# Optimization experiments

Measured on AMD Instinct MI355X. Metric: run time of the kernel, lower is better.

The kernel has to match this reference:

```python
import jax, jax.numpy as jnp
import numpy as np

B, NPG, NFEAT, NHID, NCLASS = 32, 256, 128, 64, 6
N = B * NPG
E_PER = NPG * 16
C = 1.0
SQC = 1.0  # sqrt(c)
MIN_NORM = 1e-15
PROJ_EPS = 4e-3
LAMB = 1.0


def _norm(x):
    return jnp.clip(jnp.linalg.norm(x, axis=-1, keepdims=True), MIN_NORM)


def artanh(x):
    x = jnp.clip(x, -1.0 + 1e-7, 1.0 - 1e-7)
    return 0.5 * (jnp.log1p(x) - jnp.log1p(-x))


def proj(x):
    # clip points to stay inside the Poincare ball
    n = _norm(x)
    maxn = (1.0 - PROJ_EPS) / SQC
    return jnp.where(n > maxn, x / n * maxn, x)


def expmap0(u):
    un = _norm(u)
    return jnp.tanh(SQC * un) * u / (SQC * un)


def logmap0(p):
    pn = _norm(p)
    return artanh(SQC * pn) * p / (SQC * pn)


def mobius_matvec(W, x):
    xn = _norm(x)
    mx = x @ W.T
    mxn = _norm(mx)
    return jnp.tanh(mxn / xn * artanh(SQC * xn)) * mx / (mxn * SQC)


def mobius_add(x, y):
    x2 = jnp.sum(x * x, -1, keepdims=True)
    y2 = jnp.sum(y * y, -1, keepdims=True)
    xy = jnp.sum(x * y, -1, keepdims=True)
    num = (1.0 + 2.0 * C * xy + C * y2) * x + (1.0 - C * x2) * y
    den = 1.0 + 2.0 * C * xy + C * C * x2 * y2
    return num / jnp.clip(den, MIN_NORM)


def hgc_layer(xh, adj, W, b):
    # HypLinear (mobius matvec + hyperbolic bias)
    h = proj(mobius_matvec(W, xh))
    hb = proj(expmap0(b.reshape(1, -1)))
    h = proj(mobius_add(h, hb))
    # HypAgg: aggregate in tangent space at origin
    h = proj(expmap0(adj @ logmap0(h)))
    # HypAct: relu in tangent space
    return proj(expmap0(jax.nn.relu(logmap0(h))))


def hgpsl_pool(x, adj, att, nb, npg):
    deg = adj.sum(-1)
    dis = jnp.where(deg > 0, deg ** -0.5, 0.0)
    prop = dis[:, None] * (adj @ (dis[:, None] * x))
    score = jnp.abs(x - prop).sum(-1)  # [N]
    k = npg // 2
    vals, idx = jax.lax.top_k(score.reshape(nb, npg), k)  # per-graph top-k
    gidx = (idx + (jnp.arange(nb) * npg)[:, None]).reshape(-1)  # global ids
    xn = x[gidx] * jnp.tanh(vals).reshape(-1, 1)
    adj_ind = adj[gidx][:, gidx]
    # structure learning: single-head additive attention, masked per graph
    d = xn.shape[-1]
    e = jax.nn.leaky_relu((xn @ att[:d])[:, None] + (xn @ att[d:])[None, :], 0.2)
    gid = jnp.repeat(jnp.arange(nb), k)
    mask = gid[:, None] == gid[None, :]
    new_adj = jnp.where(mask, jax.nn.relu(e) + LAMB * adj_ind, 0.0)
    return xn, new_adj


def readout(x, nb, k):
    xr = x.reshape(nb, k, -1)
    return jnp.concatenate([xr.max(axis=1), xr.mean(axis=1)], axis=-1)


def to_hyp(t):
    return proj(expmap0(t))  # proj_tan0 is identity on the Poincare ball


def forward(x, edge_index, W1, b1, W2, b2, W3, b3, att1, att2,
            lw1, lb1, lw2, lb2, lw3, lb3):
    row, col = edge_index[0], edge_index[1]
    w = (x[row].sum(-1) + x[col].sum(-1)) * 0.5
    adj1 = jnp.zeros((N, N), x.dtype).at[row, col].set(w)

    t = logmap0(hgc_layer(to_hyp(x), adj1, W1, b1))
    t, adj2 = hgpsl_pool(t, adj1, att1, B, NPG)
    k1 = NPG // 2
    x1 = readout(t, B, k1)

    t = logmap0(hgc_layer(to_hyp(t), adj2, W2, b2))
    t, adj3 = hgpsl_pool(t, adj2, att2, B, k1)
    k2 = k1 // 2
    x2 = readout(t, B, k2)

    t = logmap0(hgc_layer(to_hyp(t), adj3, W3, b3))
    x3 = readout(t, B, k2)

    r = jax.nn.relu(x1) + jax.nn.relu(x2) + jax.nn.relu(x3)
    r = jax.nn.relu(r @ lw1.T + lb1)
    r = jax.nn.relu(r @ lw2.T + lb2)
    return jax.nn.log_softmax(r @ lw3.T + lb3, axis=-1)


def setup_inputs() -> dict:
    key = jax.random.key(0)
    ks = jax.random.split(key, 16)
    s = 0.1
    x = jax.random.normal(ks[0], (N, NFEAT), jnp.float32)
    off = jnp.repeat(jnp.arange(B, dtype=jnp.int32) * NPG, E_PER)
    row = jax.random.randint(ks[1], (B * E_PER,), 0, NPG, jnp.int32) + off
    col = jax.random.randint(ks[2], (B * E_PER,), 0, NPG, jnp.int32) + off
    edge_index = jnp.stack([row, col])
    return {
        "x": x,
        "edge_index": edge_index,
        "W1": jax.random.normal(ks[3], (NHID, NFEAT), jnp.float32) * s,
        "b1": jax.random.normal(ks[4], (NHID,), jnp.float32) * s,
        "W2": jax.random.normal(ks[5], (NHID, NHID), jnp.float32) * s,
        "b2": jax.random.normal(ks[6], (NHID,), jnp.float32) * s,
        "W3": jax.random.normal(ks[7], (NHID, NHID), jnp.float32) * s,
        "b3": jax.random.normal(ks[8], (NHID,), jnp.float32) * s,
        "att1": jax.random.normal(ks[9], (2 * NHID,), jnp.float32) * s,
        "att2": jax.random.normal(ks[10], (2 * NHID,), jnp.float32) * s,
        "lw1": jax.random.normal(ks[11], (NHID, 2 * NHID), jnp.float32) * s,
        "lb1": jnp.zeros((NHID,), jnp.float32),
        "lw2": jax.random.normal(ks[12], (NHID // 2, NHID), jnp.float32) * s,
        "lb2": jnp.zeros((NHID // 2,), jnp.float32),
        "lw3": jax.random.normal(ks[13], (NCLASS, NHID // 2), jnp.float32) * s,
        "lb3": jnp.zeros((NCLASS,), jnp.float32),
    }


def reference(x, edge_index, W1, b1, W2, b2, W3, b3, att1, att2,
              lw1, lb1, lw2, lb2, lw3, lb3):
    return forward(x, edge_index, W1, b1, W2, b2, W3, b3, att1, att2,
                   lw1, lb1, lw2, lb2, lw3, lb3)
```

## Files before the change

kernel.cpp:

```cpp
#include <hip/hip_runtime.h>
#include <math.h>

#define MAXN 0.996f

__device__ __forceinline__ float wredsum(float v) {
#pragma unroll
  for (int o = 32; o > 0; o >>= 1) v += __shfl_xor(v, o);
  return v;
}

__device__ __forceinline__ float artanh_f(float x) {
  x = fminf(fmaxf(x, -1.0f + 1e-7f), 1.0f - 1e-7f);
  return 0.5f * (log1pf(x) - log1pf(-x));
}

__global__ void k_rowsum(const float* __restrict__ x, float* __restrict__ s) {
  const int row = blockIdx.x, j = threadIdx.x;
  float a = x[(size_t)row * 128 + j] + x[(size_t)row * 128 + 64 + j];
  a = wredsum(a);
  if (j == 0) s[row] = a;
}

__global__ void k_edges(const int* __restrict__ er, const int* __restrict__ ec,
                        const float* __restrict__ s, float* __restrict__ adj, int nE) {
  int e = blockIdx.x * blockDim.x + threadIdx.x;
  if (e >= nE) return;
  int r = er[e], c = ec[e];
  int g = r >> 8;
  adj[(((size_t)g * 256) + (r & 255)) * 256 + (c & 255)] = 0.5f * (s[r] + s[c]);
}

template <int IND>
__global__ void k_stageA(const float* __restrict__ x, const float* __restrict__ Wm,
                         const float* __restrict__ b, float* __restrict__ u) {
  const int row = blockIdx.x;
  const int j = threadIdx.x;
  __shared__ float xs[IND];
  for (int t = j; t < IND; t += 64) xs[t] = x[(size_t)row * IND + t];
  __syncthreads();

  float bj = b[j];
  float nb = sqrtf(wredsum(bj * bj));
  float ub = fmaxf(nb, 1e-15f);
  float eb = tanhf(ub) / ub;
  float cb = fmaxf(eb * nb, 1e-15f);
  float hbj = bj * eb * ((cb > MAXN) ? MAXN / cb : 1.0f);
  float y2 = wredsum(hbj * hbj);

  float a2 = 0.f;
  for (int t = j; t < IND; t += 64) a2 += xs[t] * xs[t];
  float nx = sqrtf(wredsum(a2));
  float un = fmaxf(nx, 1e-15f);
  float s1 = tanhf(un) / un;
  float nv = s1 * nx;
  float nn = fmaxf(nv, 1e-15f);
  float s2 = (nn > MAXN) ? MAXN / nn : 1.0f;
  float alpha = s1 * s2;
  float xn = fmaxf(fminf(nn, MAXN), 1e-15f);

  float y = 0.f;
  const float* wr = Wm + (size_t)j * IND;
  for (int t = 0; t < IND; ++t) y += xs[t] * wr[t];
  float mxj = alpha * y;
  float mxn = fmaxf(sqrtf(wredsum(mxj * mxj)), 1e-15f);
  float hj = (tanhf(mxn / xn * artanh_f(xn)) / mxn) * mxj;

  float hn = fmaxf(sqrtf(wredsum(hj * hj)), 1e-15f);
  if (hn > MAXN) hj *= MAXN / hn;

  float x2 = wredsum(hj * hj);
  float xy = wredsum(hj * hbj);
  float num = (1.f + 2.f * xy + y2) * hj + (1.f - x2) * hbj;
  float den = fmaxf(1.f + 2.f * xy + x2 * y2, 1e-15f);
  float aj = num / den;

  float an = fmaxf(sqrtf(wredsum(aj * aj)), 1e-15f);
  float pn = an;
  if (an > MAXN) { aj *= MAXN / an; pn = MAXN; }
  u[(size_t)row * 64 + j] = (artanh_f(pn) / pn) * aj;
}

template <int NPGL>
__global__ void k_stageB(const float* __restrict__ adj, const float* __restrict__ u,
                         float* __restrict__ t, float* __restrict__ dis, int wantDis) {
  const int row = blockIdx.x;
  const int g = row / NPGL;
  const int j = threadIdx.x;
  const float* arow = adj + (size_t)row * NPGL;
  const float* ug = u + (size_t)g * NPGL * 64;
  float acc = 0.f, dsum = 0.f;
  for (int c = 0; c < NPGL; ++c) { float a = arow[c]; acc += a * ug[(size_t)c * 64 + j]; dsum += a; }

  float n0 = sqrtf(wredsum(acc * acc));
  float u0 = fmaxf(n0, 1e-15f);
  float e1 = tanhf(u0) / u0;
  float c1 = fmaxf(e1 * n0, 1e-15f);
  float v = acc * e1;
  if (c1 > MAXN) { v *= MAXN / c1; c1 = MAXN; }
  v *= artanh_f(c1) / c1;
  v = fmaxf(v, 0.f);

  float n2 = sqrtf(wredsum(v * v));
  float u2 = fmaxf(n2, 1e-15f);
  float e2 = tanhf(u2) / u2;
  float c2 = fmaxf(e2 * n2, 1e-15f);
  v *= e2;
  if (c2 > MAXN) { v *= MAXN / c2; c2 = MAXN; }
  v *= artanh_f(c2) / c2;
  t[(size_t)row * 64 + j] = v;
  if (wantDis && j == 0) dis[row] = (dsum > 0.f) ? (1.0f / sqrtf(dsum)) : 0.f;
}

template <int NPGL>
__global__ void k_stageC(const float* __restrict__ adj, const float* __restrict__ t,
                         const float* __restrict__ dis, float* __restrict__ score) {
  const int row = blockIdx.x;
  const int g = row / NPGL;
  const int j = threadIdx.x;
  const float* arow = adj + (size_t)row * NPGL;
  const float* tg = t + (size_t)g * NPGL * 64;
  const float* dg = dis + (size_t)g * NPGL;
  float acc = 0.f;
  for (int c = 0; c < NPGL; ++c) acc += arow[c] * dg[c] * tg[(size_t)c * 64 + j];
  float d = fabsf(t[(size_t)row * 64 + j] - dis[row] * acc);
  d = wredsum(d);
  if (j == 0) score[row] = d;
}

template <int NPGL>
__global__ void k_stageD(const float* __restrict__ score, const float* __restrict__ t,
                         const float* __restrict__ att, float* __restrict__ xn,
                         float* __restrict__ s1o, float* __restrict__ s2o,
                         int* __restrict__ gidx, float* __restrict__ xread) {
  constexpr int K = NPGL / 2;
  const int g = blockIdx.x;
  const int i = threadIdx.x;
  __shared__ float sc[NPGL];
  __shared__ int sel[K];
  __shared__ float sval[K];
  __shared__ float xs[K * 64];
  sc[i] = score[(size_t)g * NPGL + i];
  __syncthreads();
  float si = sc[i];
  int rank = 0;
  for (int c = 0; c < NPGL; ++c) { float v = sc[c]; rank += (v > si) || (v == si && c < i); }
  if (rank < K) { sel[rank] = i; sval[rank] = si; }
  __syncthreads();
  if (i < K) {
    int li = sel[i];
    float tv = tanhf(sval[i]);
    const float* trow = t + ((size_t)g * NPGL + li) * 64;
    float a = 0.f, b = 0.f;
    for (int jj = 0; jj < 64; ++jj) {
      float v = trow[jj] * tv;
      xs[i * 64 + jj] = v;
      a += v * att[jj];
      b += v * att[64 + jj];
    }
    s1o[(size_t)g * K + i] = a;
    s2o[(size_t)g * K + i] = b;
    gidx[(size_t)g * K + i] = li;
    float* xout = xn + ((size_t)g * K + i) * 64;
    for (int jj = 0; jj < 64; ++jj) xout[jj] = xs[i * 64 + jj];
  }
  __syncthreads();
  if (i < 64) {
    float mx = -1e30f, sm = 0.f;
    for (int r = 0; r < K; ++r) { float v = xs[r * 64 + i]; mx = fmaxf(mx, v); sm += v; }
    xread[(size_t)g * 128 + i] = mx;
    xread[(size_t)g * 128 + 64 + i] = sm * (1.0f / K);
  }
}

template <int NPGL>
__global__ void k_stageE(const float* __restrict__ s1, const float* __restrict__ s2,
                         const int* __restrict__ gidx, const float* __restrict__ adj_old,
                         float* __restrict__ adj_new) {
  constexpr int K = NPGL / 2;
  int idx = blockIdx.x * blockDim.x + threadIdx.x;
  if (idx >= 32 * K * K) return;
  int g = idx / (K * K);
  int r = idx - g * K * K;
  int ii = r / K, jj = r - ii * K;
  float e = s1[(size_t)g * K + ii] + s2[(size_t)g * K + jj];
  float v = fmaxf(e, 0.f) +
            adj_old[(((size_t)g * NPGL) + gidx[(size_t)g * K + ii]) * NPGL + gidx[(size_t)g * K + jj]];
  adj_new[(((size_t)g * K) + ii) * K + jj] = v;
}

__global__ void k_readout64(const float* __restrict__ t, float* __restrict__ xread) {
  const int g = blockIdx.x, j = threadIdx.x;
  float mx = -1e30f, sm = 0.f;
  for (int r = 0; r < 64; ++r) { float v = t[((size_t)g * 64 + r) * 64 + j]; mx = fmaxf(mx, v); sm += v; }
  xread[(size_t)g * 128 + j] = mx;
  xread[(size_t)g * 128 + 64 + j] = sm * (1.0f / 64.0f);
}

__global__ void k_mlp(const float* __restrict__ x1, const float* __restrict__ x2,
                      const float* __restrict__ x3, const float* __restrict__ lw1,
                      const float* __restrict__ lb1, const float* __restrict__ lw2,
                      const float* __restrict__ lb2, const float* __restrict__ lw3,
                      const float* __restrict__ lb3, float* __restrict__ out) {
  const int b = blockIdx.x, j = threadIdx.x;
  __shared__ float r[128];
  __shared__ float h1[64];
  __shared__ float h2[32];
  __shared__ float z[6];
  for (int t = j; t < 128; t += 64)
    r[t] = fmaxf(x1[(size_t)b * 128 + t], 0.f) + fmaxf(x2[(size_t)b * 128 + t], 0.f) +
           fmaxf(x3[(size_t)b * 128 + t], 0.f);
  __syncthreads();
  float acc = lb1[j];
  for (int t = 0; t < 128; ++t) acc += r[t] * lw1[(size_t)j * 128 + t];
  h1[j] = fmaxf(acc, 0.f);
  __syncthreads();
  if (j < 32) {
    float a = lb2[j];
    for (int t = 0; t < 64; ++t) a += h1[t] * lw2[(size_t)j * 64 + t];
    h2[j] = fmaxf(a, 0.f);
  }
  __syncthreads();
  if (j < 6) {
    float a = lb3[j];
    for (int t = 0; t < 32; ++t) a += h2[t] * lw3[(size_t)j * 32 + t];
    z[j] = a;
  }
  __syncthreads();
  if (j < 6) {
    float m = z[0];
    for (int c = 1; c < 6; ++c) m = fmaxf(m, z[c]);
    float se = 0.f;
    for (int c = 0; c < 6; ++c) se += expf(z[c] - m);
    out[(size_t)b * 6 + j] = z[j] - m - logf(se);
  }
}

extern "C" void kernel_launch(void* const* d_in, const int* in_sizes, int n_in,
                              void* d_out, int out_size, void* d_ws, size_t ws_size,
                              hipStream_t stream) {
  const float* x = (const float*)d_in[0];
  const int* ei = (const int*)d_in[1];
  const float* W1 = (const float*)d_in[2];
  const float* b1 = (const float*)d_in[3];
  const float* W2 = (const float*)d_in[4];
  const float* b2 = (const float*)d_in[5];
  const float* W3 = (const float*)d_in[6];
  const float* b3 = (const float*)d_in[7];
  const float* att1 = (const float*)d_in[8];
  const float* att2 = (const float*)d_in[9];
  const float* lw1 = (const float*)d_in[10];
  const float* lb1 = (const float*)d_in[11];
  const float* lw2 = (const float*)d_in[12];
  const float* lb2 = (const float*)d_in[13];
  const float* lw3 = (const float*)d_in[14];
  const float* lb3 = (const float*)d_in[15];
  float* out = (float*)d_out;
  const int nE = in_sizes[1] / 2;

  float* p = (float*)d_ws;
  float* srow = p;  p += 8192;
  float* adj1 = p;  p += (size_t)32 * 256 * 256;
  float* adj2 = p;  p += (size_t)32 * 128 * 128;
  float* adj3 = p;  p += (size_t)32 * 64 * 64;
  float* ubuf = p;  p += (size_t)8192 * 64;
  float* t1 = p;    p += (size_t)8192 * 64;
  float* t2 = p;    p += (size_t)4096 * 64;
  float* t3 = p;    p += (size_t)2048 * 64;
  float* dis = p;   p += 8192;
  float* score = p; p += 8192;
  float* xn1 = p;   p += (size_t)4096 * 64;
  float* xn2 = p;   p += (size_t)2048 * 64;
  float* s1b = p;   p += 4096;
  float* s2b = p;   p += 4096;
  float* x1 = p;    p += 32 * 128;
  float* x2 = p;    p += 32 * 128;
  float* x3 = p;    p += 32 * 128;
  int* gidx1 = (int*)p; p += 4096;
  int* gidx2 = (int*)p; p += 2048;

  hipMemsetAsync(adj1, 0, (size_t)32 * 256 * 256 * sizeof(float), stream);
  k_rowsum<<<8192, 64, 0, stream>>>(x, srow);
  k_edges<<<(nE + 255) / 256, 256, 0, stream>>>(ei, ei + nE, srow, adj1, nE);

  k_stageA<128><<<8192, 64, 0, stream>>>(x, W1, b1, ubuf);
  k_stageB<256><<<8192, 64, 0, stream>>>(adj1, ubuf, t1, dis, 1);
  k_stageC<256><<<8192, 64, 0, stream>>>(adj1, t1, dis, score);
  k_stageD<256><<<32, 256, 0, stream>>>(score, t1, att1, xn1, s1b, s2b, gidx1, x1);
  k_stageE<256><<<(32 * 128 * 128 + 255) / 256, 256, 0, stream>>>(s1b, s2b, gidx1, adj1, adj2);

  k_stageA<64><<<4096, 64, 0, stream>>>(xn1, W2, b2, ubuf);
  k_stageB<128><<<4096, 64, 0, stream>>>(adj2, ubuf, t2, dis, 1);
  k_stageC<128><<<4096, 64, 0, stream>>>(adj2, t2, dis, score);
  k_stageD<128><<<32, 128, 0, stream>>>(score, t2, att2, xn2, s1b, s2b, gidx2, x2);
  k_stageE<128><<<(32 * 64 * 64 + 255) / 256, 256, 0, stream>>>(s1b, s2b, gidx2, adj2, adj3);

  k_stageA<64><<<2048, 64, 0, stream>>>(xn2, W3, b3, ubuf);
  k_stageB<64><<<2048, 64, 0, stream>>>(adj3, ubuf, t3, dis, 0);
  k_readout64<<<32, 64, 0, stream>>>(t3, x3);

  k_mlp<<<32, 64, 0, stream>>>(x1, x2, x3, lw1, lb1, lw2, lb2, lw3, lb3, out);
}
```

Before: 257.4 us.

## Tile GCN stages across multiple rows per block with shared-memory reuse

Stages A, B and C now process several rows per 256-thread block instead of one row per 64-thread block. Weights and adjacency rows are staged in shared memory so each loaded column of u/t is reused across 4 rows. The bias expmap is precomputed once in a separate kernel, and dis-scaled t is written in stage B so stage C skips the per-column dis multiply. This cuts redundant global reads of the node features, at the cost of an extra workspace buffer and an extra tiny launch.

```diff
diff --git a/kernel.cpp b/kernel.cpp
--- a/kernel.cpp
+++ b/kernel.cpp
@@ -14,8 +14,27 @@
   return 0.5f * (log1pf(x) - log1pf(-x));
 }
 
+__global__ void k_prebias(const float* __restrict__ b1, const float* __restrict__ b2,
+                          const float* __restrict__ b3, float* __restrict__ hbA,
+                          float* __restrict__ y2A) {
+  const int j = threadIdx.x;
+  const float* bs[3] = {b1, b2, b3};
+  for (int l = 0; l < 3; ++l) {
+    float bj = bs[l][j];
+    float nb = sqrtf(wredsum(bj * bj));
+    float ub = fmaxf(nb, 1e-15f);
+    float eb = tanhf(ub) / ub;
+    float cb = fmaxf(eb * nb, 1e-15f);
+    float hbj = bj * eb * ((cb > MAXN) ? MAXN / cb : 1.0f);
+    hbA[l * 64 + j] = hbj;
+    float y2 = wredsum(hbj * hbj);
+    if (j == 0) y2A[l] = y2;
+  }
+}
+
 __global__ void k_rowsum(const float* __restrict__ x, float* __restrict__ s) {
-  const int row = blockIdx.x, j = threadIdx.x;
+  const int w = threadIdx.x >> 6, j = threadIdx.x & 63;
+  const int row = blockIdx.x * 4 + w;
   float a = x[(size_t)row * 128 + j] + x[(size_t)row * 128 + 64 + j];
   a = wredsum(a);
   if (j == 0) s[row] = a;
@@ -31,100 +50,172 @@
 }
 
 template <int IND>
-__global__ void k_stageA(const float* __restrict__ x, const float* __restrict__ Wm,
-                         const float* __restrict__ b, float* __restrict__ u) {
-  const int row = blockIdx.x;
-  const int j = threadIdx.x;
-  __shared__ float xs[IND];
-  for (int t = j; t < IND; t += 64) xs[t] = x[(size_t)row * IND + t];
-  __syncthreads();
-
-  float bj = b[j];
-  float nb = sqrtf(wredsum(bj * bj));
-  float ub = fmaxf(nb, 1e-15f);
-  float eb = tanhf(ub) / ub;
-  float cb = fmaxf(eb * nb, 1e-15f);
-  float hbj = bj * eb * ((cb > MAXN) ? MAXN / cb : 1.0f);
-  float y2 = wredsum(hbj * hbj);
-
-  float a2 = 0.f;
-  for (int t = j; t < IND; t += 64) a2 += xs[t] * xs[t];
-  float nx = sqrtf(wredsum(a2));
-  float un = fmaxf(nx, 1e-15f);
-  float s1 = tanhf(un) / un;
-  float nv = s1 * nx;
-  float nn = fmaxf(nv, 1e-15f);
-  float s2 = (nn > MAXN) ? MAXN / nn : 1.0f;
-  float alpha = s1 * s2;
-  float xn = fmaxf(fminf(nn, MAXN), 1e-15f);
-
-  float y = 0.f;
-  const float* wr = Wm + (size_t)j * IND;
-  for (int t = 0; t < IND; ++t) y += xs[t] * wr[t];
-  float mxj = alpha * y;
-  float mxn = fmaxf(sqrtf(wredsum(mxj * mxj)), 1e-15f);
-  float hj = (tanhf(mxn / xn * artanh_f(xn)) / mxn) * mxj;
-
-  float hn = fmaxf(sqrtf(wredsum(hj * hj)), 1e-15f);
-  if (hn > MAXN) hj *= MAXN / hn;
-
-  float x2 = wredsum(hj * hj);
-  float xy = wredsum(hj * hbj);
-  float num = (1.f + 2.f * xy + y2) * hj + (1.f - x2) * hbj;
-  float den = fmaxf(1.f + 2.f * xy + x2 * y2, 1e-15f);
-  float aj = num / den;
-
-  float an = fmaxf(sqrtf(wredsum(aj * aj)), 1e-15f);
-  float pn = an;
-  if (an > MAXN) { aj *= MAXN / an; pn = MAXN; }
-  u[(size_t)row * 64 + j] = (artanh_f(pn) / pn) * aj;
+__global__ __launch_bounds__(256) void k_stageA(const float* __restrict__ x,
+                                                const float* __restrict__ Wm,
+                                                const float* __restrict__ hb,
+                                                const float* __restrict__ y2p,
+                                                float* __restrict__ u) {
+  constexpr int WSTR = IND + 4;
+  __shared__ float Wl[64 * WSTR];
+  __shared__ float xsh[8 * IND];
+  const int tid = threadIdx.x;
+  const int w = tid >> 6, j = tid & 63;
+  const int rowBase = blockIdx.x * 8;
+
+  for (int f = tid; f < 64 * IND; f += 256) {
+    int jj = f / IND, t = f - jj * IND;
+    Wl[jj * WSTR + t] = Wm[f];
+  }
+  for (int f = tid; f < 8 * IND; f += 256) xsh[f] = x[(size_t)rowBase * IND + f];
+  __syncthreads();
+
+  const float hbj = hb[j];
+  const float y2 = y2p[0];
+  const float4* wrow = (const float4*)(Wl + j * WSTR);
+
+#pragma unroll
+  for (int rr = 0; rr < 2; ++rr) {
+    const int lr = w * 2 + rr;
+    const float* xs = xsh + lr * IND;
+
+    float a2 = 0.f;
+#pragma unroll
+    for (int t = j; t < IND; t += 64) a2 += xs[t] * xs[t];
+    float nx = sqrtf(wredsum(a2));
+    float un = fmaxf(nx, 1e-15f);
+    float s1 = tanhf(un) / un;
+    float nv = s1 * nx;
+    float nn = fmaxf(nv, 1e-15f);
+    float s2 = (nn > MAXN) ? MAXN / nn : 1.0f;
+    float alpha = s1 * s2;
+    float xn = fmaxf(fminf(nn, MAXN), 1e-15f);
+
+    const float4* xv4 = (const float4*)xs;
+    float y = 0.f;
+#pragma unroll
+    for (int t4 = 0; t4 < IND / 4; ++t4) {
+      float4 w4 = wrow[t4];
+      float4 v4 = xv4[t4];
+      y += w4.x * v4.x + w4.y * v4.y + w4.z * v4.z + w4.w * v4.w;
+    }
+    float mxj = alpha * y;
+    float mxn = fmaxf(sqrtf(wredsum(mxj * mxj)), 1e-15f);
+    float hj = (tanhf(mxn / xn * artanh_f(xn)) / mxn) * mxj;
+
+    float hn = fmaxf(sqrtf(wredsum(hj * hj)), 1e-15f);
+    if (hn > MAXN) hj *= MAXN / hn;
+
+    float x2 = wredsum(hj * hj);
+    float xy = wredsum(hj * hbj);
+    float num = (1.f + 2.f * xy + y2) * hj + (1.f - x2) * hbj;
+    float den = fmaxf(1.f + 2.f * xy + x2 * y2, 1e-15f);
+    float aj = num / den;
+
+    float an = fmaxf(sqrtf(wredsum(aj * aj)), 1e-15f);
+    float pn = an;
+    if (an > MAXN) { aj *= MAXN / an; pn = MAXN; }
+    u[((size_t)rowBase + lr) * 64 + j] = (artanh_f(pn) / pn) * aj;
+  }
 }
 
 template <int NPGL>
-__global__ void k_stageB(const float* __restrict__ adj, const float* __restrict__ u,
-                         float* __restrict__ t, float* __restrict__ dis, int wantDis) {
-  const int row = blockIdx.x;
-  const int g = row / NPGL;
-  const int j = threadIdx.x;
-  const float* arow = adj + (size_t)row * NPGL;
+__global__ __launch_bounds__(256) void k_stageB(const float* __restrict__ adj,
+                                                const float* __restrict__ u,
+                                                float* __restrict__ t,
+                                                float* __restrict__ dt,
+                                                float* __restrict__ dis, int wantDis) {
+  __shared__ float adjl[16 * NPGL];
+  const int tid = threadIdx.x;
+  const int w = tid >> 6, j = tid & 63;
+  const int rowBase = blockIdx.x * 16;
+  const int g = rowBase / NPGL;
+  for (int f = tid; f < 16 * NPGL; f += 256) adjl[f] = adj[(size_t)rowBase * NPGL + f];
+  __syncthreads();
   const float* ug = u + (size_t)g * NPGL * 64;
-  float acc = 0.f, dsum = 0.f;
-  for (int c = 0; c < NPGL; ++c) { float a = arow[c]; acc += a * ug[(size_t)c * 64 + j]; dsum += a; }
-
-  float n0 = sqrtf(wredsum(acc * acc));
-  float u0 = fmaxf(n0, 1e-15f);
-  float e1 = tanhf(u0) / u0;
-  float c1 = fmaxf(e1 * n0, 1e-15f);
-  float v = acc * e1;
-  if (c1 > MAXN) { v *= MAXN / c1; c1 = MAXN; }
-  v *= artanh_f(c1) / c1;
-  v = fmaxf(v, 0.f);
-
-  float n2 = sqrtf(wredsum(v * v));
-  float u2 = fmaxf(n2, 1e-15f);
-  float e2 = tanhf(u2) / u2;
-  float c2 = fmaxf(e2 * n2, 1e-15f);
-  v *= e2;
-  if (c2 > MAXN) { v *= MAXN / c2; c2 = MAXN; }
-  v *= artanh_f(c2) / c2;
-  t[(size_t)row * 64 + j] = v;
-  if (wantDis && j == 0) dis[row] = (dsum > 0.f) ? (1.0f / sqrtf(dsum)) : 0.f;
+
+  float acc[4] = {0.f, 0.f, 0.f, 0.f};
+  for (int c4 = 0; c4 < NPGL / 4; ++c4) {
+    const int c = c4 * 4;
+    float u0 = ug[(size_t)(c + 0) * 64 + j];
+    float u1 = ug[(size_t)(c + 1) * 64 + j];
+    float u2 = ug[(size_t)(c + 2) * 64 + j];
+    float u3 = ug[(size_t)(c + 3) * 64 + j];
+#pragma unroll
+    for (int r = 0; r < 4; ++r) {
+      float4 a4 = *(const float4*)&adjl[(w * 4 + r) * NPGL + c];
+      acc[r] += a4.x * u0 + a4.y * u1 + a4.z * u2 + a4.w * u3;
+    }
+  }
+
+#pragma unroll
+  for (int r = 0; r < 4; ++r) {
+    const int lr = w * 4 + r;
+    const int row = rowBase + lr;
+    float ds = 0.f;
+    for (int c = j; c < NPGL; c += 64) ds += adjl[lr * NPGL + c];
+    ds = wredsum(ds);
+    float disr = (ds > 0.f) ? (1.0f / sqrtf(ds)) : 0.f;
+
+    float v = acc[r];
+    float n0 = sqrtf(wredsum(v * v));
+    float u0 = fmaxf(n0, 1e-15f);
+    float e1 = tanhf(u0) / u0;
+    float c1 = fmaxf(e1 * n0, 1e-15f);
+    v *= e1;
+    if (c1 > MAXN) { v *= MAXN / c1; c1 = MAXN; }
+    v *= artanh_f(c1) / c1;
+    v = fmaxf(v, 0.f);
+
+    float n2 = sqrtf(wredsum(v * v));
+    float u2m = fmaxf(n2, 1e-15f);
+    float e2 = tanhf(u2m) / u2m;
+    float c2 = fmaxf(e2 * n2, 1e-15f);
+    v *= e2;
+    if (c2 > MAXN) { v *= MAXN / c2; c2 = MAXN; }
+    v *= artanh_f(c2) / c2;
+    t[(size_t)row * 64 + j] = v;
+    if (wantDis) {
+      dt[(size_t)row * 64 + j] = disr * v;
+      if (j == 0) dis[row] = disr;
+    }
+  }
 }
 
 template <int NPGL>
-__global__ void k_stageC(const float* __restrict__ adj, const float* __restrict__ t,
-                         const float* __restrict__ dis, float* __restrict__ score) {
-  const int row = blockIdx.x;
-  const int g = row / NPGL;
-  const int j = threadIdx.x;
-  const float* arow = adj + (size_t)row * NPGL;
-  const float* tg = t + (size_t)g * NPGL * 64;
-  const float* dg = dis + (size_t)g * NPGL;
-  float acc = 0.f;
-  for (int c = 0; c < NPGL; ++c) acc += arow[c] * dg[c] * tg[(size_t)c * 64 + j];
-  float d = fabsf(t[(size_t)row * 64 + j] - dis[row] * acc);
-  d = wredsum(d);
-  if (j == 0) score[row] = d;
+__global__ __launch_bounds__(256) void k_stageC(const float* __restrict__ adj,
+                                                const float* __restrict__ t,
+                                                const float* __restrict__ dt,
+                                                const float* __restrict__ dis,
+                                                float* __restrict__ score) {
+  __shared__ float adjl[16 * NPGL];
+  const int tid = threadIdx.x;
+  const int w = tid >> 6, j = tid & 63;
+  const int rowBase = blockIdx.x * 16;
+  const int g = rowBase / NPGL;
+  for (int f = tid; f < 16 * NPGL; f += 256) adjl[f] = adj[(size_t)rowBase * NPGL + f];
+  __syncthreads();
+  const float* dtg = dt + (size_t)g * NPGL * 64;
+
+  float acc[4] = {0.f, 0.f, 0.f, 0.f};
+  for (int c4 = 0; c4 < NPGL / 4; ++c4) {
+    const int c = c4 * 4;
+    float u0 = dtg[(size_t)(c + 0) * 64 + j];
+    float u1 = dtg[(size_t)(c + 1) * 64 + j];
+    float u2 = dtg[(size_t)(c + 2) * 64 + j];
+    float u3 = dtg[(size_t)(c + 3) * 64 + j];
+#pragma unroll
+    for (int r = 0; r < 4; ++r) {
+      float4 a4 = *(const float4*)&adjl[(w * 4 + r) * NPGL + c];
+      acc[r] += a4.x * u0 + a4.y * u1 + a4.z * u2 + a4.w * u3;
+    }
+  }
+#pragma unroll
+  for (int r = 0; r < 4; ++r) {
+    const int row = rowBase + w * 4 + r;
+    float d = fabsf(t[(size_t)row * 64 + j] - dis[row] * acc[r]);
+    d = wredsum(d);
+    if (j == 0) score[row] = d;
+  }
 }
 
 template <int NPGL>
@@ -266,6 +357,7 @@
   float* t1 = p;    p += (size_t)8192 * 64;
   float* t2 = p;    p += (size_t)4096 * 64;
   float* t3 = p;    p += (size_t)2048 * 64;
+  float* dtb = p;   p += (size_t)8192 * 64;
   float* dis = p;   p += 8192;
   float* score = p; p += 8192;
   float* xn1 = p;   p += (size_t)4096 * 64;
@@ -275,27 +367,30 @@
   float* x1 = p;    p += 32 * 128;
   float* x2 = p;    p += 32 * 128;
   float* x3 = p;    p += 32 * 128;
+  float* hbA = p;   p += 3 * 64;
+  float* y2A = p;   p += 16;
   int* gidx1 = (int*)p; p += 4096;
   int* gidx2 = (int*)p; p += 2048;
 
   hipMemsetAsync(adj1, 0, (size_t)32 * 256 * 256 * sizeof(float), stream);
-  k_rowsum<<<8192, 64, 0, stream>>>(x, srow);
+  k_prebias<<<1, 64, 0, stream>>>(b1, b2, b3, hbA, y2A);
+  k_rowsum<<<2048, 256, 0, stream>>>(x, srow);
   k_edges<<<(nE + 255) / 256, 256, 0, stream>>>(ei, ei + nE, srow, adj1, nE);
 
-  k_stageA<128><<<8192, 64, 0, stream>>>(x, W1, b1, ubuf);
-  k_stageB<256><<<8192, 64, 0, stream>>>(adj1, ubuf, t1, dis, 1);
-  k_stageC<256><<<8192, 64, 0, stream>>>(adj1, t1, dis, score);
+  k_stageA<128><<<1024, 256, 0, stream>>>(x, W1, hbA, y2A, ubuf);
+  k_stageB<256><<<512, 256, 0, stream>>>(adj1, ubuf, t1, dtb, dis, 1);
+  k_stageC<256><<<512, 256, 0, stream>>>(adj1, t1, dtb, dis, score);
   k_stageD<256><<<32, 256, 0, stream>>>(score, t1, att1, xn1, s1b, s2b, gidx1, x1);
   k_stageE<256><<<(32 * 128 * 128 + 255) / 256, 256, 0, stream>>>(s1b, s2b, gidx1, adj1, adj2);
 
-  k_stageA<64><<<4096, 64, 0, stream>>>(xn1, W2, b2, ubuf);
-  k_stageB<128><<<4096, 64, 0, stream>>>(adj2, ubuf, t2, dis, 1);
-  k_stageC<128><<<4096, 64, 0, stream>>>(adj2, t2, dis, score);
+  k_stageA<64><<<512, 256, 0, stream>>>(xn1, W2, hbA + 64, y2A + 1, ubuf);
+  k_stageB<128><<<256, 256, 0, stream>>>(adj2, ubuf, t2, dtb, dis, 1);
+  k_stageC<128><<<256, 256, 0, stream>>>(adj2, t2, dtb, dis, score);
   k_stageD<128><<<32, 128, 0, stream>>>(score, t2, att2, xn2, s1b, s2b, gidx2, x2);
   k_stageE<128><<<(32 * 64 * 64 + 255) / 256, 256, 0, stream>>>(s1b, s2b, gidx2, adj2, adj3);
 
-  k_stageA<64><<<2048, 64, 0, stream>>>(xn2, W3, b3, ubuf);
-  k_stageB<64><<<2048, 64, 0, stream>>>(adj3, ubuf, t3, dis, 0);
+  k_stageA<64><<<256, 256, 0, stream>>>(xn2, W3, hbA + 128, y2A + 2, ubuf);
+  k_stageB<64><<<128, 256, 0, stream>>>(adj3, ubuf, t3, dtb, dis, 0);
   k_readout64<<<32, 64, 0, stream>>>(t3, x3);
 
   k_mlp<<<32, 64, 0, stream>>>(x1, x2, x3, lw1, lb1, lw2, lb2, lw3, lb3, out);
```

Result: slower. 272.5 us (+5.9%).
